# Performance work log

Measured on AMD Instinct MI355X. Metric: run time of the kernel, lower is better.

The kernel has to match this reference:

```python
import jax, jax.numpy as jnp
import numpy as np

N = 100000          # num nodes
E = 1600000         # num edges (before self loops)
IN_C = 128
OUT_C = 64
RATIO = 0.5
NEG_SLOPE = 0.2


def setup_inputs() -> dict:
    key = jax.random.key(0)
    k1, k2, k3, k4, k5 = jax.random.split(key, 5)
    x = jax.random.normal(k1, (N, IN_C), jnp.float32)
    # edges with no self loops (module removes then re-adds self loops)
    src = jax.random.randint(k2, (E,), 0, N, dtype=jnp.int32)
    off = jax.random.randint(k3, (E,), 1, N, dtype=jnp.int32)
    tgt = (src + off) % N
    edge_index = jnp.stack([src, tgt])  # [2, E], row0=source(j), row1=target(i)
    # glorot init
    s_w = float(np.sqrt(6.0 / (IN_C + OUT_C)))
    weight = jax.random.uniform(k4, (IN_C, OUT_C), jnp.float32, -s_w, s_w)
    s_a = float(np.sqrt(6.0 / (1 + 2 * OUT_C)))
    att = jax.random.uniform(k5, (1, 2 * OUT_C), jnp.float32, -s_a, s_a)
    batch = jnp.zeros((N,), jnp.int32)  # single graph
    return {"x": x, "weight": weight, "att": att,
            "edge_index": edge_index, "batch": batch, "bn": 0}


def reference(x, weight, att, edge_index, batch, bn):
    # add self loops (static shapes: E + N edges)
    loops = jnp.arange(N, dtype=edge_index.dtype)
    src = jnp.concatenate([edge_index[0], loops])  # edge_index_j (source)
    tgt = jnp.concatenate([edge_index[1], loops])  # edge_index_i (target)

    h = x @ weight                      # [N, OUT_C]
    x_j = h[src]                        # [E+N, OUT_C] gathered source feats
    x_i = h[tgt]

    # alpha = (cat([x_i, x_j]) * att).sum(-1)
    alpha = x_i @ att[0, :OUT_C] + x_j @ att[0, OUT_C:]   # [E+N]
    alpha = jnp.where(alpha > 0, alpha, NEG_SLOPE * alpha)  # leaky_relu

    # edge-softmax grouped by target node (every node has a self loop -> no empty segment)
    m = jax.ops.segment_max(alpha, tgt, num_segments=N)
    a = jnp.exp(alpha - m[tgt])
    denom = jax.ops.segment_sum(a, tgt, num_segments=N)
    alpha = a / (denom[tgt] + 1e-16)

    # node importance = sum of attention over outgoing edges (grouped by source)
    alpha_sum = jax.ops.segment_sum(alpha, src, num_segments=N)

    # topk node selection (ratio of all nodes; single graph)
    k = int(np.ceil(RATIO * N))
    _, topk_idx = jax.lax.top_k(alpha_sum, k)
    node_mask = jnp.zeros((N,), bool).at[topk_idx].set(True)

    # filter_dn: keep edges whose both endpoints survive; mask instead of compacting
    edge_mask = node_mask[src] & node_mask[tgt]
    alpha_m = jnp.where(edge_mask, alpha, 0.0)

    # weighted scatter-add aggregation to target nodes (aggr='add')
    out = jax.ops.segment_sum(alpha_m[:, None] * x_j, tgt, num_segments=N)  # [N, OUT_C]
    # bn flag is 0 -> BatchNorm skipped
    return out, edge_mask, node_mask
```

## Files before the change

### kernel.cpp

```cpp
#include <hip/hip_runtime.h>
#include <stdint.h>

#define IN_C 128
#define OUT_C 64
#define NEG_SLOPE 0.2f
#define RB 256
#define PTPB 1024
#define RBINS 512
#define SCAP 5120
#define SGRID (RBINS * SCAP)
#define KC 8
#define SXW 192

typedef unsigned int u32;
typedef unsigned char u8;
typedef unsigned long long u64;

__device__ __forceinline__ u32 fenc(float f) {
  u32 u = __float_as_uint(f);
  return (u & 0x80000000u) ? ~u : (u | 0x80000000u);
}
__device__ __forceinline__ u64 key64(float v, int i) {
  return (((u64)fenc(v)) << 32) | (u64)(0xffffffffu - (u32)i);
}

__global__ __launch_bounds__(128) void k_gemm(const float* __restrict__ x,
                                              const float* __restrict__ w,
                                              const float* __restrict__ att,
                                              float* __restrict__ h,
                                              float* __restrict__ ai, float* __restrict__ aj,
                                              int N) {
  __shared__ float swc[KC * OUT_C];
  __shared__ float sx[KC * SXW];
  int tid = threadIdx.x;
  int rbase = blockIdx.x * 128;

  int c0 = (tid & 7) * 8;
  int rg = tid >> 3;
  int sxbase = rg * 12;
  float acc[8][8];
#pragma unroll
  for (int i = 0; i < 8; i++)
#pragma unroll
    for (int j = 0; j < 8; j++) acc[i][j] = 0.f;

  int grow = rbase + tid;
  int base = (tid >> 3) * 12 + (tid & 7);
  const float* xp = &x[(size_t)grow * IN_C];

  int wr = tid >> 4;
  int wc4 = (tid & 15) * 4;
  const float* wp = &w[(size_t)wr * OUT_C + wc4];

  float4 pv0 = make_float4(0.f, 0.f, 0.f, 0.f);
  float4 pv1 = make_float4(0.f, 0.f, 0.f, 0.f);
  if (grow < N) {
    pv0 = *(const float4*)&xp[0];
    pv1 = *(const float4*)&xp[4];
  }
  float4 pw = *(const float4*)&wp[0];

  for (int kb = 0; kb < IN_C; kb += KC) {
    __syncthreads();
    sx[0 * SXW + base] = pv0.x;
    sx[1 * SXW + base] = pv0.y;
    sx[2 * SXW + base] = pv0.z;
    sx[3 * SXW + base] = pv0.w;
    sx[4 * SXW + base] = pv1.x;
    sx[5 * SXW + base] = pv1.y;
    sx[6 * SXW + base] = pv1.z;
    sx[7 * SXW + base] = pv1.w;
    *(float4*)&swc[wr * OUT_C + wc4] = pw;
    if (kb + KC < IN_C) {
      pw = *(const float4*)&wp[(size_t)(kb + KC) * OUT_C];
      if (grow < N) {
        pv0 = *(const float4*)&xp[kb + KC];
        pv1 = *(const float4*)&xp[kb + KC + 4];
      }
    }
    __syncthreads();
#pragma unroll
    for (int kl = 0; kl < KC; ++kl) {
      float xr[8], wv[8];
      *(float4*)&xr[0] = *(const float4*)&sx[kl * SXW + sxbase];
      *(float4*)&xr[4] = *(const float4*)&sx[kl * SXW + sxbase + 4];
      *(float4*)&wv[0] = *(const float4*)&swc[kl * OUT_C + c0];
      *(float4*)&wv[4] = *(const float4*)&swc[kl * OUT_C + c0 + 4];
#pragma unroll
      for (int i = 0; i < 8; ++i)
#pragma unroll
        for (int j = 0; j < 8; ++j)
          acc[i][j] += xr[i] * wv[j];
    }
  }

  float pi[8], pj[8];
#pragma unroll
  for (int i = 0; i < 8; ++i) { pi[i] = 0.f; pj[i] = 0.f; }
#pragma unroll
  for (int j = 0; j < 8; ++j) {
    float a0 = att[c0 + j], a1 = att[OUT_C + c0 + j];
#pragma unroll
    for (int i = 0; i < 8; ++i) {
      pi[i] += acc[i][j] * a0;
      pj[i] += acc[i][j] * a1;
    }
  }
#pragma unroll
  for (int o = 1; o < 8; o <<= 1) {
#pragma unroll
    for (int i = 0; i < 8; ++i) {
      pi[i] += __shfl_xor(pi[i], o);
      pj[i] += __shfl_xor(pj[i], o);
    }
  }
#pragma unroll
  for (int i = 0; i < 8; ++i) {
    int row = rbase + rg * 8 + i;
    if (row < N) {
      *(float4*)&h[(size_t)row * OUT_C + c0]     = make_float4(acc[i][0], acc[i][1], acc[i][2], acc[i][3]);
      *(float4*)&h[(size_t)row * OUT_C + c0 + 4] = make_float4(acc[i][4], acc[i][5], acc[i][6], acc[i][7]);
      if ((tid & 7) == 0) { ai[row] = pi[i]; aj[row] = pj[i]; }
    }
  }
}

__global__ __launch_bounds__(1024) void k_part_t(const int* __restrict__ src, const int* __restrict__ tgt,
                                                 const float* __restrict__ aj,
                                                 int E, int EN, int chunk,
                                                 u32* __restrict__ gcurT, u64* __restrict__ bufS,
                                                 u32* __restrict__ sel, u32 kSel) {
  __shared__ u32 lh[RBINS];
  __shared__ u32 cur[RBINS];
  int tid = threadIdx.x, b = blockIdx.x;
  if (b == 0 && tid == 0) { sel[0] = 0u; sel[1] = 0u; sel[2] = kSel; sel[3] = 0u; }
  for (int d = tid; d < RBINS; d += PTPB) lh[d] = 0u;
  __syncthreads();
  int lo = b * chunk, hi = min(lo + chunk, EN);
  for (int e = lo + tid; e < hi; e += PTPB) {
    int t = (e < E) ? tgt[e] : e - E;
    atomicAdd(&lh[((u32)t) >> 8], 1u);
  }
  __syncthreads();
  for (int d = tid; d < RBINS; d += PTPB) {
    u32 c = lh[d];
    cur[d] = c ? (u32)(d * SCAP) + atomicAdd(&gcurT[d], c) : 0u;
  }
  __syncthreads();
  for (int e = lo + tid; e < hi; e += PTPB) {
    int s, t;
    if (e < E) { s = src[e]; t = tgt[e]; } else { s = t = e - E; }
    u32 tb = ((u32)t) >> 8;
    u32 p = atomicAdd(&cur[tb], 1u);
    if (p < (tb + 1u) * SCAP) {
      float av = aj[s];
      bufS[p] = (((u64)((((u32)t & 255u) << 24) | (u32)s)) << 32) | (u64)__float_as_uint(av);
    }
  }
}

__global__ __launch_bounds__(256) void k_rpass2(const u64* __restrict__ in, u32* __restrict__ out,
                                                const u32* __restrict__ gcurT, u32* __restrict__ gcurS,
                                                u32* __restrict__ offT,
                                                const float* __restrict__ ai,
                                                float* __restrict__ alpha,
                                                u64* __restrict__ pv,
                                                int N) {
  __shared__ u32 hist[256];
  __shared__ u32 sc[256];
  __shared__ u32 lhs[RBINS];
  __shared__ u32 stage[SCAP];
  __shared__ float stageV[SCAP];
  int tid = threadIdx.x, d = blockIdx.x;
  u32 start = (u32)(d * SCAP);
  u32 cntb = min(gcurT[d], (u32)SCAP);
  u32 end = start + cntb;
  int sz = (int)cntb;
  hist[tid] = 0u;
  for (int dd = tid; dd < RBINS; dd += 256) lhs[dd] = 0u;
  __syncthreads();
  for (u32 p = start + tid; p < end; p += 256) {
    u32 it = (u32)(in[p] >> 32);
    atomicAdd(&hist[it >> 24], 1u);
    atomicAdd(&lhs[(it & 0xffffffu) >> 8], 1u);
  }
  __syncthreads();
  for (int dd = tid; dd < RBINS; dd += 256) {
    u32 c = lhs[dd];
    lhs[dd] = c ? (u32)(dd * SCAP) + atomicAdd(&gcurS[dd], c) : 0u;
  }
  u32 hv = hist[tid];
  sc[tid] = hv;
  __syncthreads();
  for (int o = 1; o < 256; o <<= 1) {
    u32 t = (tid >= o) ? sc[tid - o] : 0u;
    __syncthreads();
    sc[tid] += t;
    __syncthreads();
  }
  u32 excl = sc[tid] - hv;
  int node = (d << 8) + tid;
  if (node < N) offT[node] = start + excl;
  if (node == N - 1) offT[N] = start + sc[tid];
  hist[tid] = excl;
  __syncthreads();
  for (u32 p = start + tid; p < end; p += 256) {
    u64 it64 = in[p];
    u32 it = (u32)(it64 >> 32);
    u32 lp = atomicAdd(&hist[it >> 24], 1u);
    stage[lp] = it;
    stageV[lp] = __uint_as_float((u32)it64);
  }
  __syncthreads();
  for (int i = tid; i < sz; i += 256) out[start + i] = stage[i];
  if (node < N) {
    int lb = (tid > 0) ? (int)sc[tid - 1] : 0;
    int le = (int)sc[tid];
    float an = ai[node];
    float mx = -1e30f;
    for (int i = lb; i < le; ++i) {
      float a = an + stageV[i];
      a = a > 0.f ? a : NEG_SLOPE * a;
      stageV[i] = a;
      mx = fmaxf(mx, a);
    }
    float sm = 0.f;
    for (int i = lb; i < le; ++i) {
      float v = expf(stageV[i] - mx);
      stageV[i] = v;
      sm += v;
    }
    float inv = 1.f / (sm + 1e-16f);
    for (int i = lb; i < le; ++i) {
      float vn = stageV[i] * inv;
      stageV[i] = vn;
      alpha[start + i] = vn;
    }
  }
  __syncthreads();
  for (u32 p = start + tid; p < end; p += 256) {
    int i = (int)(p - start);
    u32 sp = stage[i] & 0xffffffu;
    u32 sb = sp >> 8;
    u32 pos = atomicAdd(&lhs[sb], 1u);
    if (pos < (sb + 1u) * SCAP)
      pv[pos] = (((u64)(sp & 255u)) << 32) | (u64)__float_as_uint(stageV[i]);
  }
}

__global__ __launch_bounds__(256) void k_asum_acc(const u64* __restrict__ pv,
                                                  const u32* __restrict__ gcurS,
                                                  float* __restrict__ asum,
                                                  u32* __restrict__ hist8, u32* __restrict__ done,
                                                  u32* __restrict__ sel, int N, int nblk) {
  __shared__ float sums[256];
  __shared__ u32 lh[256];
  __shared__ u32 s[256];
  __shared__ u32 sres;
  int tid = threadIdx.x, d = blockIdx.x;
  u32 start = (u32)(d * SCAP);
  u32 end = start + min(gcurS[d], (u32)SCAP);
  sums[tid] = 0.f;
  __syncthreads();
  for (u32 p = start + tid; p < end; p += 256) {
    u64 it = pv[p];
    atomicAdd(&sums[(u32)(it >> 32)], __uint_as_float((u32)it));
  }
  __syncthreads();
  int node = d * 256 + tid;
  u32 bin = 256u;
  if (node < N) {
    float v = sums[tid];
    asum[node] = v;
    bin = (u32)(key64(v, node) >> 56) & 255u;
  }
  lh[tid] = 0u;
  __syncthreads();
  if (bin < 256u) atomicAdd(&lh[bin], 1u);
  __syncthreads();
  if (lh[tid]) atomicAdd(&hist8[tid], lh[tid]);
  __syncthreads();
  if (tid == 0)
    sres = __hip_atomic_fetch_add(&done[0], 1u, __ATOMIC_ACQ_REL, __HIP_MEMORY_SCOPE_AGENT);
  __syncthreads();
  if (sres == (u32)(nblk - 1)) {
    u32 krem = sel[2];
    u32 hv = __hip_atomic_load(&hist8[255 - tid], __ATOMIC_RELAXED, __HIP_MEMORY_SCOPE_AGENT);
    s[tid] = hv;
    __syncthreads();
    for (int o = 1; o < 256; o <<= 1) {
      u32 t = (tid >= o) ? s[tid - o] : 0u;
      __syncthreads();
      s[tid] += t;
      __syncthreads();
    }
    u32 cum = s[tid], prev = (tid > 0) ? s[tid - 1] : 0u;
    if (cum >= krem && prev < krem) {
      ((u64*)sel)[0] = (u64)(u32)(255 - tid);
      sel[2] = krem - prev;
    }
  }
}

__global__ __launch_bounds__(256) void k_histpick(const float* __restrict__ asum,
                                                  u32* __restrict__ list_out, u32* __restrict__ cnt_out,
                                                  u32* __restrict__ hist8, u32* __restrict__ done,
                                                  u32* __restrict__ sel, int N, int nblk) {
  __shared__ u32 lh[256];
  __shared__ u32 sres;
  __shared__ u32 s[256];
  int tid = threadIdx.x;
  lh[tid] = 0u;
  __syncthreads();
  u64 prefix = ((const u64*)sel)[0];
  int i = blockIdx.x * 256 + tid;
  if (i < N) {
    u64 k = key64(asum[i], i);
    if ((k >> 56) == prefix) {
      atomicAdd(&lh[(u32)(k >> 48) & 255u], 1u);
      u32 p = atomicAdd(cnt_out, 1u);
      list_out[p] = (u32)i;
    }
  }
  __syncthreads();
  if (lh[tid]) atomicAdd(&hist8[256 + tid], lh[tid]);
  __syncthreads();
  if (tid == 0)
    sres = __hip_atomic_fetch_add(&done[1], 1u, __ATOMIC_ACQ_REL, __HIP_MEMORY_SCOPE_AGENT);
  __syncthreads();
  if (sres == (u32)(nblk - 1)) {
    u32 krem = sel[2];
    u32 hv = __hip_atomic_load(&hist8[256 + (255 - tid)], __ATOMIC_RELAXED,
                               __HIP_MEMORY_SCOPE_AGENT);
    s[tid] = hv;
    __syncthreads();
    for (int o = 1; o < 256; o <<= 1) {
      u32 t = (tid >= o) ? s[tid - o] : 0u;
      __syncthreads();
      s[tid] += t;
      __syncthreads();
    }
    u32 cum = s[tid], prev = (tid > 0) ? s[tid - 1] : 0u;
    if (cum >= krem && prev < krem) {
      ((u64*)sel)[0] = (prefix << 8) | (u64)(u32)(255 - tid);
      sel[2] = krem - prev;
    }
  }
}

__global__ __launch_bounds__(256) void k_histpick_final(const float* __restrict__ asum,
                                                        const u32* __restrict__ list_in, const u32* __restrict__ cnt_in,
                                                        u32* __restrict__ list_out, u32* __restrict__ cnt_out,
                                                        u32* __restrict__ hist8, u32* __restrict__ done,
                                                        u32* __restrict__ sel, int nblk) {
  __shared__ u32 lh[256];
  __shared__ u32 s[256];
  __shared__ u32 sres;
  __shared__ u64 keys[2048];
  __shared__ u32 cc;
  __shared__ u64 sprefix;
  __shared__ u32 skrem;
  int tid = threadIdx.x;
  lh[tid] = 0u;
  __syncthreads();
  u64 prefix = ((const u64*)sel)[0];
  u32 n = *cnt_in;
  u32 i = blockIdx.x * 256 + tid;
  if (i < n) {
    int idx = (int)list_in[i];
    u64 k = key64(asum[idx], idx);
    if ((k >> 48) == prefix) {
      atomicAdd(&lh[(u32)(k >> 40) & 255u], 1u);
      u32 p = atomicAdd(cnt_out, 1u);
      list_out[p] = (u32)idx;
    }
  }
  __syncthreads();
  if (lh[tid]) atomicAdd(&hist8[512 + tid], lh[tid]);
  __syncthreads();
  if (tid == 0)
    sres = __hip_atomic_fetch_add(&done[2], 1u, __ATOMIC_ACQ_REL, __HIP_MEMORY_SCOPE_AGENT);
  __syncthreads();
  if (sres != (u32)(nblk - 1)) return;
  u32 krem = sel[2];
  u32 hv = __hip_atomic_load(&hist8[512 + (255 - tid)], __ATOMIC_RELAXED, __HIP_MEMORY_SCOPE_AGENT);
  s[tid] = hv;
  __syncthreads();
  for (int o = 1; o < 256; o <<= 1) {
    u32 t = (tid >= o) ? s[tid - o] : 0u;
    __syncthreads();
    s[tid] += t;
    __syncthreads();
  }
  {
    u32 cum = s[tid], prev = (tid > 0) ? s[tid - 1] : 0u;
    if (cum >= krem && prev < krem) { sprefix = (prefix << 8) | (u64)(u32)(255 - tid); skrem = krem - prev; }
  }
  __syncthreads();
  u64 pfx3 = sprefix;
  u32 krem3 = skrem;
  u32 n3 = *cnt_out;
  lh[tid] = 0u;
  __syncthreads();
  for (u32 j = tid; j < n3; j += 256) {
    int idx = (int)list_out[j];
    u64 k = key64(asum[idx], idx);
    if ((k >> 40) == pfx3) atomicAdd(&lh[(u32)(k >> 32) & 255u], 1u);
  }
  __syncthreads();
  s[tid] = lh[255 - tid];
  __syncthreads();
  for (int o = 1; o < 256; o <<= 1) {
    u32 t = (tid >= o) ? s[tid - o] : 0u;
    __syncthreads();
    s[tid] += t;
    __syncthreads();
  }
  {
    u32 cum = s[tid], prev = (tid > 0) ? s[tid - 1] : 0u;
    if (cum >= krem3 && prev < krem3) { sprefix = (pfx3 << 8) | (u64)(u32)(255 - tid); skrem = krem3 - prev; }
  }
  if (tid == 0) cc = 0u;
  __syncthreads();
  u32 fsel = (u32)sprefix;
  u32 kremF = skrem;
  for (u32 j = tid; j < n3; j += 256) {
    int idx = (int)list_out[j];
    u64 k = key64(asum[idx], idx);
    if ((u32)(k >> 32) == fsel) {
      u32 p = atomicAdd(&cc, 1u);
      if (p < 2048) keys[p] = k;
    }
  }
  __syncthreads();
  int C = (int)min(cc, 2048u);
  for (int j = tid; j < C; j += 256) {
    u64 k = keys[j];
    u32 rank = 0;
    for (int q = 0; q < C; ++q)
      if (keys[q] > k) rank++;
    if (rank == kremF - 1) ((u64*)sel)[0] = k;
  }
}

__global__ __launch_bounds__(256) void k_node_mask(const float* __restrict__ asum,
                                                   const u32* __restrict__ sel,
                                                   u32* __restrict__ nm,
                                                   float* __restrict__ out_node, int N) {
  int i = blockIdx.x * 256 + threadIdx.x;
  if (i >= N) return;
  u64 T = ((const u64*)sel)[0];
  bool m = key64(asum[i], i) >= T;
  nm[i] = m ? 1u : 0u;
  out_node[i] = m ? 1.f : 0.f;
}

__global__ __launch_bounds__(256) void k_mask(const int* __restrict__ src, const int* __restrict__ tgt,
                                              const u32* __restrict__ nm,
                                              const u32* __restrict__ csr, const float* __restrict__ alpha,
                                              const u32* __restrict__ gcurT,
                                              float* __restrict__ out_edge, u64* __restrict__ pair,
                                              int E, int EN) {
  int q = blockIdx.x * 256 + threadIdx.x;
  if (q < EN) {
    int s, t;
    if (q < E) { s = src[q]; t = tgt[q]; } else { s = t = q - E; }
    out_edge[q] = (nm[s] && nm[t]) ? 1.f : 0.f;
  }
  if (q < SGRID) {
    u32 b = (u32)q / (u32)SCAP;
    u32 r = (u32)q - b * (u32)SCAP;
    if (r < min(gcurT[b], (u32)SCAP)) {
      u32 sp = csr[q] & 0xffffffu;
      u32 ab = nm[sp] ? __float_as_uint(alpha[q]) : 0u;
      pair[q] = (((u64)sp) << 32) | ab;
    }
  }
}

__global__ __launch_bounds__(256) void k_aggregate(const u32* __restrict__ off,
                                                   const u64* __restrict__ pair,
                                                   const float* __restrict__ h,
                                                   const u32* __restrict__ nm,
                                                   const u32* __restrict__ gcurT,
                                                   float* __restrict__ out, int N) {
  int node = blockIdx.x * 4 + (threadIdx.x >> 6);
  int lane = threadIdx.x & 63;
  int g = lane >> 4;
  int c = lane & 15;
  if (node >= N) return;
  float4 acc = make_float4(0.f, 0.f, 0.f, 0.f);
  if (nm[node]) {
    u32 bkt = (u32)node >> 8;
    u32 bend = bkt * (u32)SCAP + min(gcurT[bkt], (u32)SCAP);
    u32 b = off[node];
    u32 e2 = min(off[node + 1], bend);
    for (u32 p0 = b; p0 < e2; p0 += 32) {
      u64 pr[8];
      float av[8];
      u32 sv[8];
#pragma unroll
      for (int q = 0; q < 8; ++q) {
        u32 p = p0 + q * 4 + (u32)g;
        bool ok = p < e2;
        pr[q] = pair[ok ? p : b];
        av[q] = ok ? __uint_as_float((u32)pr[q]) : 0.f;
        sv[q] = (u32)(pr[q] >> 32);
      }
      float4 hv[8];
#pragma unroll
      for (int q = 0; q < 8; ++q) {
        hv[q] = make_float4(0.f, 0.f, 0.f, 0.f);
        if (av[q] != 0.f)
          hv[q] = *(const float4*)&h[(size_t)sv[q] * OUT_C + c * 4];
      }
#pragma unroll
      for (int q = 0; q < 8; ++q) {
        acc.x += av[q] * hv[q].x;
        acc.y += av[q] * hv[q].y;
        acc.z += av[q] * hv[q].z;
        acc.w += av[q] * hv[q].w;
      }
    }
#pragma unroll
    for (int o = 16; o < 64; o <<= 1) {
      acc.x += __shfl_xor(acc.x, o);
      acc.y += __shfl_xor(acc.y, o);
      acc.z += __shfl_xor(acc.z, o);
      acc.w += __shfl_xor(acc.w, o);
    }
  }
  if (g == 0)
    *(float4*)&out[(size_t)node * OUT_C + c * 4] = acc;
}

extern "C" void kernel_launch(void* const* d_in, const int* in_sizes, int n_in,
                              void* d_out, int out_size, void* d_ws, size_t ws_size,
                              hipStream_t stream) {
  const float* x   = (const float*)d_in[0];
  const float* w   = (const float*)d_in[1];
  const float* att = (const float*)d_in[2];
  const int*   ei  = (const int*)d_in[3];

  int N = in_sizes[0] / IN_C;
  int E = in_sizes[3] / 2;
  int EN = E + N;
  const int* src = ei;
  const int* tgt = ei + E;

  float* out      = (float*)d_out;
  float* out_edge = out + (size_t)N * OUT_C;
  float* out_node = out_edge + (size_t)EN;

  char* p = (char*)d_ws;
  auto alloc = [&](size_t bytes) -> char* {
    char* r = p;
    p += (bytes + 255) & ~(size_t)255;
    return r;
  };
  float* h     = (float*)alloc((size_t)N * OUT_C * 4);
  float* ai    = (float*)alloc((size_t)N * 4);
  float* aj    = (float*)alloc((size_t)N * 4);
  u64*   stg   = (u64*)alloc((size_t)SGRID * 8);
  u32*   bufA  = (u32*)alloc((size_t)SGRID * 4);
  float* alpha = (float*)alloc((size_t)SGRID * 4);
  u64*   pv    = (u64*)alloc((size_t)SGRID * 8);
  u32*   offT  = (u32*)alloc((size_t)(N + 1) * 4);
  float* asum  = (float*)alloc((size_t)N * 4);
  u32*   nm    = (u32*)alloc((size_t)N * 4);
  u32*   listA = (u32*)alloc((size_t)N * 4);
  u32*   listB = (u32*)alloc((size_t)N * 4);
  u32*   zb    = (u32*)alloc((RBINS + RBINS + 2048 + 8 + 8) * 4);
  u32*   gcurT = zb;
  u32*   gcurS = zb + RBINS;
  u32*   hist8 = zb + 2 * RBINS;
  u32*   done  = zb + 2 * RBINS + 2048;
  u32*   cnt   = zb + 2 * RBINS + 2048 + 8;
  u32*   sel   = (u32*)alloc(256);

  u64*   pair  = pv;

  u32 kSel = (u32)((N + 1) / 2);
  int chunk = (EN + RB - 1) / RB;
  int gGemm = (N + 127) / 128;
  int gN = (N + 255) / 256;
  int gS = (SGRID + 255) / 256;
  int gNode4 = (N + 3) / 4;

  hipMemsetAsync(zb, 0, (RBINS + RBINS + 2048 + 8 + 8) * 4, stream);

  k_gemm<<<gGemm, 128, 0, stream>>>(x, w, att, h, ai, aj, N);

  k_part_t<<<RB, PTPB, 0, stream>>>(src, tgt, aj, E, EN, chunk, gcurT, stg, sel, kSel);
  k_rpass2<<<RBINS, 256, 0, stream>>>(stg, bufA, gcurT, gcurS, offT, ai, alpha, pv, N);
  k_asum_acc<<<RBINS, 256, 0, stream>>>(pv, gcurS, asum, hist8, done, sel, N, RBINS);

  k_histpick<<<gN, 256, 0, stream>>>(asum, listA, &cnt[1], hist8, done, sel, N, gN);
  k_histpick_final<<<gN, 256, 0, stream>>>(asum, listA, &cnt[1], listB, &cnt[2],
                                           hist8, done, sel, gN);

  k_node_mask<<<gN, 256, 0, stream>>>(asum, sel, nm, out_node, N);
  k_mask<<<gS, 256, 0, stream>>>(src, tgt, nm, bufA, alpha, gcurT, out_edge, pair, E, EN);
  k_aggregate<<<gNode4, 256, 0, stream>>>(offT, pair, h, nm, gcurT, out, N);
}
```

Measured before the change: 315.8 us.

## Compact selected nodes into a list and aggregate only over surviving nodes

The node-mask kernel now appends each selected node to a compacted list through an atomic counter and writes zero rows of the output directly for unselected nodes. Aggregation launches only over the selected nodes instead of all nodes, which removes idle wavefronts for the half that are masked out. The edge-pair build also skips edges whose target node is not selected, and the histogram pass loads only the high 32-bit word of each key. The list order is nondeterministic because of the atomic append, and the grid size assumes exactly kSel nodes are selected, so ties in the selection threshold could leave some rows unwritten.

```diff
diff --git a/kernel.cpp b/kernel.cpp
--- a/kernel.cpp
+++ b/kernel.cpp
@@ -179,10 +179,13 @@
   hist[tid] = 0u;
   for (int dd = tid; dd < RBINS; dd += 256) lhs[dd] = 0u;
   __syncthreads();
-  for (u32 p = start + tid; p < end; p += 256) {
-    u32 it = (u32)(in[p] >> 32);
-    atomicAdd(&hist[it >> 24], 1u);
-    atomicAdd(&lhs[(it & 0xffffffu) >> 8], 1u);
+  {
+    const u32* inHi = ((const u32*)in) + 1;
+    for (u32 p = start + tid; p < end; p += 256) {
+      u32 it = inHi[2 * (size_t)p];
+      atomicAdd(&hist[it >> 24], 1u);
+      atomicAdd(&lhs[(it & 0xffffffu) >> 8], 1u);
+    }
   }
   __syncthreads();
   for (int dd = tid; dd < RBINS; dd += 256) {
@@ -446,13 +449,24 @@
 __global__ __launch_bounds__(256) void k_node_mask(const float* __restrict__ asum,
                                                    const u32* __restrict__ sel,
                                                    u32* __restrict__ nm,
-                                                   float* __restrict__ out_node, int N) {
+                                                   float* __restrict__ out_node,
+                                                   u32* __restrict__ slist, u32* __restrict__ scnt,
+                                                   float* __restrict__ out, int N) {
   int i = blockIdx.x * 256 + threadIdx.x;
   if (i >= N) return;
   u64 T = ((const u64*)sel)[0];
   bool m = key64(asum[i], i) >= T;
   nm[i] = m ? 1u : 0u;
   out_node[i] = m ? 1.f : 0.f;
+  if (m) {
+    u32 p = atomicAdd(scnt, 1u);
+    slist[p] = (u32)i;
+  } else {
+    float4 z = make_float4(0.f, 0.f, 0.f, 0.f);
+    float4* o = (float4*)&out[(size_t)i * OUT_C];
+#pragma unroll
+    for (int q = 0; q < 16; ++q) o[q] = z;
+  }
 }
 
 __global__ __launch_bounds__(256) void k_mask(const int* __restrict__ src, const int* __restrict__ tgt,
@@ -471,9 +485,13 @@
     u32 b = (u32)q / (u32)SCAP;
     u32 r = (u32)q - b * (u32)SCAP;
     if (r < min(gcurT[b], (u32)SCAP)) {
-      u32 sp = csr[q] & 0xffffffu;
-      u32 ab = nm[sp] ? __float_as_uint(alpha[q]) : 0u;
-      pair[q] = (((u64)sp) << 32) | ab;
+      u32 it = csr[q];
+      u32 tnode = (b << 8) + (it >> 24);
+      if (nm[tnode]) {
+        u32 sp = it & 0xffffffu;
+        u32 ab = nm[sp] ? __float_as_uint(alpha[q]) : 0u;
+        pair[q] = (((u64)sp) << 32) | ab;
+      }
     }
   }
 }
@@ -481,16 +499,17 @@
 __global__ __launch_bounds__(256) void k_aggregate(const u32* __restrict__ off,
                                                    const u64* __restrict__ pair,
                                                    const float* __restrict__ h,
-                                                   const u32* __restrict__ nm,
+                                                   const u32* __restrict__ slist,
                                                    const u32* __restrict__ gcurT,
-                                                   float* __restrict__ out, int N) {
-  int node = blockIdx.x * 4 + (threadIdx.x >> 6);
+                                                   float* __restrict__ out, int kSel) {
+  int idx = blockIdx.x * 4 + (threadIdx.x >> 6);
   int lane = threadIdx.x & 63;
   int g = lane >> 4;
   int c = lane & 15;
-  if (node >= N) return;
+  if (idx >= kSel) return;
+  int node = (int)slist[idx];
   float4 acc = make_float4(0.f, 0.f, 0.f, 0.f);
-  if (nm[node]) {
+  {
     u32 bkt = (u32)node >> 8;
     u32 bend = bkt * (u32)SCAP + min(gcurT[bkt], (u32)SCAP);
     u32 b = off[node];
@@ -570,6 +589,7 @@
   u32*   nm    = (u32*)alloc((size_t)N * 4);
   u32*   listA = (u32*)alloc((size_t)N * 4);
   u32*   listB = (u32*)alloc((size_t)N * 4);
+  u32*   slist = (u32*)alloc((size_t)N * 4);
   u32*   zb    = (u32*)alloc((RBINS + RBINS + 2048 + 8 + 8) * 4);
   u32*   gcurT = zb;
   u32*   gcurS = zb + RBINS;
@@ -585,7 +605,7 @@
   int gGemm = (N + 127) / 128;
   int gN = (N + 255) / 256;
   int gS = (SGRID + 255) / 256;
-  int gNode4 = (N + 3) / 4;
+  int gAgg = (int)((kSel + 3) / 4);
 
   hipMemsetAsync(zb, 0, (RBINS + RBINS + 2048 + 8 + 8) * 4, stream);
 
@@ -599,7 +619,7 @@
   k_histpick_final<<<gN, 256, 0, stream>>>(asum, listA, &cnt[1], listB, &cnt[2],
                                            hist8, done, sel, gN);
 
-  k_node_mask<<<gN, 256, 0, stream>>>(asum, sel, nm, out_node, N);
+  k_node_mask<<<gN, 256, 0, stream>>>(asum, sel, nm, out_node, slist, &cnt[4], out, N);
   k_mask<<<gS, 256, 0, stream>>>(src, tgt, nm, bufA, alpha, gcurT, out_edge, pair, E, EN);
-  k_aggregate<<<gNode4, 256, 0, stream>>>(offT, pair, h, nm, gcurT, out, N);
-}
+  k_aggregate<<<gAgg, 256, 0, stream>>>(offT, pair, h, slist, gcurT, out, (int)kSel);
+}
```

After: 330.4 us. 4.6% more time.
